# Optimization experiments

Hardware: AMD Instinct MI355X
Metric: run time of the kernel (lower is better)

Reference implementation:

```python
import jax, jax.numpy as jnp
import numpy as np
from jax import lax

NLAT_IN, NLON_IN = 480, 960
NLAT_OUT, NLON_OUT = 721, 1440
KSIZE = 9      # morlet basis: prod(kernel_shape) = 3*3
NNZ = 20       # sparse quadrature entries per output latitude row
C_IN, C_OUT = 32, 32
BATCH = 1


def setup_inputs() -> dict:
    key = jax.random.key(0)
    k1, k2, k3, k4, k5 = jax.random.split(key, 5)
    x = jax.random.normal(k1, (BATCH, C_IN, NLAT_IN, NLON_IN), dtype=jnp.float32)
    weight = jax.random.normal(k2, (C_OUT, C_IN, KSIZE), dtype=jnp.float32) * 0.05
    # sparse DISCO quadrature values (quadrature weights folded in)
    psi_vals = jax.random.uniform(k3, (KSIZE, NLAT_OUT, NNZ), dtype=jnp.float32) / NNZ
    # geodesic neighborhood: latitude rows within +-2 of output row, small lon offsets
    ho = jnp.arange(NLAT_OUT, dtype=jnp.int32)[:, None]
    psi_hi = jnp.clip(ho + jax.random.randint(k4, (NLAT_OUT, NNZ), -2, 3, dtype=jnp.int32), 0, NLAT_OUT - 1)
    psi_dw = jax.random.randint(k5, (NLAT_OUT, NNZ), -10, 11, dtype=jnp.int32) % NLON_OUT
    return {"x": x, "weight": weight, "psi_vals": psi_vals, "psi_hi": psi_hi, "psi_dw": psi_dw}


def _resample_s2(x, h_out, w_out):
    """Bilinear lat interpolation + periodic linear lon interpolation (ResampleS2)."""
    b, c, h, w = x.shape
    # latitude: both grids are linspace(0, pi, nlat) equiangular
    pos_h = jnp.linspace(0.0, float(h - 1), h_out)
    h0 = jnp.clip(jnp.floor(pos_h).astype(jnp.int32), 0, h - 2)
    fh = (pos_h - h0.astype(jnp.float32)).astype(x.dtype)
    x = x[:, :, h0, :] * (1.0 - fh)[None, None, :, None] + x[:, :, h0 + 1, :] * fh[None, None, :, None]
    # longitude: periodic, lon_j = 2*pi*j/nlon
    pos_w = jnp.arange(w_out, dtype=jnp.float32) * (w / w_out)
    w0 = jnp.floor(pos_w).astype(jnp.int32)
    fw = (pos_w - w0.astype(jnp.float32)).astype(x.dtype)
    w0 = w0 % w
    w1 = (w0 + 1) % w
    return x[..., w0] * (1.0 - fw) + x[..., w1] * fw


def _disco_conv(x, weight, psi_vals, psi_hi, psi_dw):
    """Sparse discrete-continuous spherical conv (gather -> basis weight -> channel mix).
    psi is stored for longitude 0 and applied with a periodic longitude shift."""
    b, c, h, w = x.shape  # [B, Cin, 721, 1440]
    o = weight.shape[0]
    wo = jnp.arange(w, dtype=jnp.int32)

    def body(acc, inp):
        v, hi, dw = inp  # v: [K, Hout], hi/dw: [Hout]
        cols = (dw[:, None] + wo[None, :]) % w          # [Hout, W]
        g = x[:, :, hi[:, None], cols]                  # gather -> [B, Cin, Hout, W]
        weff = jnp.einsum("ock,kh->och", weight, v)     # fold basis into channel mix
        return acc + jnp.einsum("och,bchw->bohw", weff, g), None

    acc0 = jnp.zeros((b, o, h, w), dtype=x.dtype)
    scan_in = (jnp.moveaxis(psi_vals, 2, 0), psi_hi.T, psi_dw.T)  # leading axis NNZ
    acc, _ = lax.scan(body, acc0, scan_in)
    return acc


def reference(x, weight, psi_vals, psi_hi, psi_dw):
    x = _resample_s2(x, NLAT_OUT, NLON_OUT)
    return _disco_conv(x, weight, psi_vals, psi_hi, psi_dw)
```

## Files before the change

kernel.cpp:

```cpp
#include <hip/hip_runtime.h>
#include <hip/hip_bf16.h>

#define NLAT_IN  480
#define NLON_IN  960
#define NLAT_OUT 721
#define NLON_OUT 1440
#define KSIZE    9
#define NNZ      20
#define CH       32

typedef __bf16 bf16x8 __attribute__((ext_vector_type(8)));
typedef float  f32x4  __attribute__((ext_vector_type(4)));
typedef unsigned u32x4 __attribute__((ext_vector_type(4)));

__device__ __forceinline__ unsigned short f2bf(float f) {
    unsigned u = __float_as_uint(f);
    u += 0x7fffu + ((u >> 16) & 1u);
    return (unsigned short)(u >> 16);
}

#define W_TILE   180
#define IN_LD4   31
#define LDS_PITCH 129

__global__ __launch_bounds__(256) void resample_kernel(
        const float* __restrict__ x,
        unsigned short* __restrict__ xr) {
    __shared__ float ld[2 * CH * LDS_PITCH];

    int h  = blockIdx.y;
    int bx = blockIdx.x;
    int wb = bx * W_TILE;
    int base_in = bx * (W_TILE * 2 / 3);

    float pos_h = (float)h * (479.0f / 720.0f);
    int h0 = (int)floorf(pos_h);
    if (h0 < 0) h0 = 0;
    if (h0 > NLAT_IN - 2) h0 = NLAT_IN - 2;
    float fh = pos_h - (float)h0;

    const int t = threadIdx.x;
    for (int i = 0; i < 8; ++i) {
        int lin = i * 256 + t;
        if (lin < 2 * CH * IN_LD4) {
            int r   = lin / (CH * IN_LD4);
            int rem = lin - r * (CH * IN_LD4);
            int c   = rem / IN_LD4;
            int j   = rem - c * IN_LD4;
            int src = base_in + 4 * j;
            if (src >= NLON_IN) src -= NLON_IN;
            f32x4 v = *(const f32x4*)(x + ((size_t)c * NLAT_IN + h0 + r) * NLON_IN + src);
            float* dst = ld + (r * CH + c) * LDS_PITCH + 4 * j;
            dst[0] = v.x; dst[1] = v.y; dst[2] = v.z; dst[3] = v.w;
        }
    }
    __syncthreads();

    float ifh = 1.0f - fh;
    for (int i = 0; i < 3; ++i) {
        int d = i * 256 + t;
        if (d >= W_TILE * (CH / 8)) break;
        int w_l = d >> 2;
        int cg  = d & 3;
        int w = wb + w_l;
        float pos_w = (float)w * ((float)NLON_IN / (float)NLON_OUT);
        int w0 = (int)floorf(pos_w);
        float fw = pos_w - (float)w0;
        int wl0 = w0 - base_in;
        float ifw = 1.0f - fw;

        unsigned rr[4];
#pragma unroll
        for (int j = 0; j < 4; ++j) {
            int c = cg * 8 + j * 2;
            const float* r0 = ld + c * LDS_PITCH + wl0;
            const float* r1 = r0 + CH * LDS_PITCH;
            float v0 = ifh * (ifw * r0[0] + fw * r0[1]) + fh * (ifw * r1[0] + fw * r1[1]);
            const float* q0 = r0 + LDS_PITCH;
            const float* q1 = r1 + LDS_PITCH;
            float v1 = ifh * (ifw * q0[0] + fw * q0[1]) + fh * (ifw * q1[0] + fw * q1[1]);
            rr[j] = (unsigned)f2bf(v0) | ((unsigned)f2bf(v1) << 16);
        }
        u32x4 uv; uv[0] = rr[0]; uv[1] = rr[1]; uv[2] = rr[2]; uv[3] = rr[3];
        *(u32x4*)((unsigned*)xr + ((size_t)h * NLON_OUT + w) * (CH / 2) + cg * 4) = uv;
    }
}

__global__ __launch_bounds__(256) void weff_kernel(
        const float* __restrict__ weight,
        const float* __restrict__ psi_vals,
        unsigned short* __restrict__ weff) {
    __shared__ float wl[KSIZE * CH * CH];

    const int t = threadIdx.x;
    for (int i = 0; i < 9; ++i) {
        int lin = i * 256 + t;
        if (lin < KSIZE * CH * CH / 4) {
            f32x4 v = *(const f32x4*)(weight + lin * 4);
            float vv[4] = {v.x, v.y, v.z, v.w};
#pragma unroll
            for (int q = 0; q < 4; ++q) {
                int l4 = lin * 4 + q;
                int k  = l4 % KSIZE;
                int occ = l4 / KSIZE;
                wl[k * (CH * CH) + occ] = vv[q];
            }
        }
    }
    __syncthreads();

    int hnz = blockIdx.x * 16 + (t >> 4);
    int cp  = t & 15;
    if (hnz >= NLAT_OUT * NNZ) return;

    float p[KSIZE];
#pragma unroll
    for (int k = 0; k < KSIZE; ++k)
        p[k] = psi_vals[(size_t)k * (NLAT_OUT * NNZ) + hnz];

    unsigned* outp = (unsigned*)weff + (size_t)hnz * (CH * CH / 2) + cp;
#pragma unroll 4
    for (int oc = 0; oc < CH; ++oc) {
        float a0 = 0.f, a1 = 0.f;
        const float* wb = wl + oc * CH + cp * 2;
#pragma unroll
        for (int k = 0; k < KSIZE; ++k) {
            a0 += wb[k * (CH * CH)]     * p[k];
            a1 += wb[k * (CH * CH) + 1] * p[k];
        }
        outp[oc * 16] = (unsigned)f2bf(a0) | ((unsigned)f2bf(a1) << 16);
    }
}

#define ST_ROWS 8
#define ST_COLS 128
#define HBLK4   181
#define NPAIRD  (HBLK4 * 15)
#define PER_XCD ((NPAIRD + 7) / 8)

__global__ __launch_bounds__(512, 4) void disco_kernel(
        const unsigned short* __restrict__ xr,
        const unsigned short* __restrict__ weff,
        const int* __restrict__ psi_hi,
        const int* __restrict__ psi_dw,
        float* __restrict__ out) {
    __shared__ unsigned short st[ST_ROWS * ST_COLS * CH];

    int bid = blockIdx.x;
    int xcd = bid & 7;
    int p   = xcd * PER_XCD + (bid >> 3);
    if (p >= NPAIRD) return;
    int hblk = p / 15;
    int wblk = p - hblk * 15;
    int h0        = hblk * 4;
    int wbase_blk = wblk * 96;

    int wave = threadIdx.x >> 6;
    int lane = threadIdx.x & 63;
    int l15  = lane & 15;
    int quad = lane >> 4;
    int c0   = quad * 8;
    int jh   = wave >> 1;
    int wq   = wave & 1;

    int  h  = h0 + jh;
    bool hv = (h < NLAT_OUT);

    int swz = ((lane >> 2) << 5) + (((lane & 3) ^ ((lane >> 3) & 3)) << 3);

    const unsigned short* weff_h = weff + (size_t)h * (NNZ * CH * CH);
    const int* hip_ = psi_hi + h * NNZ;
    const int* dwp  = psi_dw + h * NNZ;

    bf16x8 pa0[2], pa1[2];
    int phi[2], pdw[2];
    if (hv) {
#pragma unroll
        for (int q = 0; q < 2; ++q) {
            const unsigned short* wp = weff_h + q * (CH * CH);
            pa0[q] = *(const bf16x8*)(wp + l15 * CH + c0);
            pa1[q] = *(const bf16x8*)(wp + (16 + l15) * CH + c0);
            phi[q] = hip_[q];
            pdw[q] = dwp[q];
        }
    }

    int cstart = wbase_blk - 16;
    if (cstart < 0) cstart += NLON_OUT;
    for (int i = wave; i < ST_ROWS * (ST_COLS / 16); i += 8) {
        int r  = i >> 3;
        int ck = i & 7;
        int gh = h0 - 2 + r;
        gh = gh < 0 ? 0 : (gh > NLAT_OUT - 1 ? NLAT_OUT - 1 : gh);
        int gc = cstart + ck * 16;
        if (gc >= NLON_OUT) gc -= NLON_OUT;
        const unsigned short* gp = xr + ((size_t)gh * NLON_OUT + gc) * CH + swz;
        unsigned short* lp = st + (r * ST_COLS + ck * 16) * CH;
        __builtin_amdgcn_global_load_lds(
            (const __attribute__((address_space(1))) void*)gp,
            (__attribute__((address_space(3))) void*)lp, 16, 0, 0);
    }
    __syncthreads();

    if (hv) {
        f32x4 acc[2][3] = {};
        int wcol0 = 16 + wq * 48 + l15;

#pragma unroll
        for (int nz = 0; nz < NNZ; ++nz) {
            const int sl = nz & 1;
            bf16x8 a0 = pa0[sl];
            bf16x8 a1 = pa1[sl];
            int hi = phi[sl];
            int dw = pdw[sl];
            if (nz + 2 < NNZ) {
                const unsigned short* wp = weff_h + (nz + 2) * (CH * CH);
                pa0[sl] = *(const bf16x8*)(wp + l15 * CH + c0);
                pa1[sl] = *(const bf16x8*)(wp + (16 + l15) * CH + c0);
                phi[sl] = hip_[nz + 2];
                pdw[sl] = dwp[nz + 2];
            }
            int shift = dw > 720 ? dw - NLON_OUT : dw;
            int rloc  = hi - h0 + 2;
            int cbase = wcol0 + shift;
            int sel   = ((((cbase >> 1) & 3) ^ quad) << 3);
            const unsigned short* bp =
                st + (size_t)rloc * (ST_COLS * CH) + cbase * CH + sel;
#pragma unroll
            for (int s = 0; s < 3; ++s) {
                bf16x8 b = *(const bf16x8*)(bp + s * 16 * CH);
                acc[0][s] = __builtin_amdgcn_mfma_f32_16x16x32_bf16(a0, b, acc[0][s], 0, 0, 0);
                acc[1][s] = __builtin_amdgcn_mfma_f32_16x16x32_bf16(a1, b, acc[1][s], 0, 0, 0);
            }
        }

#pragma unroll
        for (int hh = 0; hh < 2; ++hh)
#pragma unroll
            for (int s = 0; s < 3; ++s)
#pragma unroll
                for (int r = 0; r < 4; ++r) {
                    int oc = hh * 16 + quad * 4 + r;
                    int w  = wbase_blk + wq * 48 + s * 16 + l15;
                    out[((size_t)oc * NLAT_OUT + h) * NLON_OUT + w] = acc[hh][s][r];
                }
    }
}

extern "C" void kernel_launch(void* const* d_in, const int* in_sizes, int n_in,
                              void* d_out, int out_size, void* d_ws, size_t ws_size,
                              hipStream_t stream) {
    const float* x        = (const float*)d_in[0];
    const float* weight   = (const float*)d_in[1];
    const float* psi_vals = (const float*)d_in[2];
    const int*   psi_hi   = (const int*)d_in[3];
    const int*   psi_dw   = (const int*)d_in[4];
    float* out = (float*)d_out;

    unsigned short* xr = (unsigned short*)d_ws;
    unsigned short* wf = (unsigned short*)((char*)d_ws + (size_t)NLAT_OUT * NLON_OUT * CH * 2);

    {
        dim3 grid(NLON_OUT / W_TILE, NLAT_OUT);
        resample_kernel<<<grid, 256, 0, stream>>>(x, xr);
    }
    {
        int nblk = (NLAT_OUT * NNZ + 15) / 16;
        weff_kernel<<<nblk, 256, 0, stream>>>(weight, psi_vals, wf);
    }
    {
        disco_kernel<<<8 * PER_XCD, 512, 0, stream>>>(xr, wf, psi_hi, psi_dw, out);
    }
}
```

Measured before the change: 305.6 us.

## Merge resample and weff kernels; shrink disco tile to 48 columns with deeper prefetch

Merges the resample and weff precompute kernels into one launch, with block-index ranges selecting the role. This removes one kernel launch and its tail. The disco kernel now uses 256-thread blocks that each cover 48 longitude columns and 4 latitude rows, with a smaller 80-column LDS stage, so there are more, smaller blocks. The weff/psi register prefetch depth goes from 2 to 4 and is issued before the barrier so it overlaps the LDS fill. The cost is more halo reloading per output column (80 staged columns for 48 outputs instead of 128 for 96) and higher register pressure.

```diff
diff --git a/kernel.cpp b/kernel.cpp
--- a/kernel.cpp
+++ b/kernel.cpp
@@ -22,14 +22,66 @@
 #define W_TILE   180
 #define IN_LD4   31
 #define LDS_PITCH 129
-
-__global__ __launch_bounds__(256) void resample_kernel(
+#define NBLK_WEFF 902
+#define NBLK_RES  (8 * NLAT_OUT)
+
+__global__ __launch_bounds__(256) void pre_kernel(
         const float* __restrict__ x,
-        unsigned short* __restrict__ xr) {
-    __shared__ float ld[2 * CH * LDS_PITCH];
-
-    int h  = blockIdx.y;
-    int bx = blockIdx.x;
+        const float* __restrict__ weight,
+        const float* __restrict__ psi_vals,
+        unsigned short* __restrict__ xr,
+        unsigned short* __restrict__ weff) {
+    __shared__ float smem[KSIZE * CH * CH];
+
+    const int bid = blockIdx.x;
+    const int t   = threadIdx.x;
+
+    if (bid < NBLK_WEFF) {
+        float* wl = smem;
+        for (int i = 0; i < 9; ++i) {
+            int lin = i * 256 + t;
+            if (lin < KSIZE * CH * CH / 4) {
+                f32x4 v = *(const f32x4*)(weight + lin * 4);
+                float vv[4] = {v.x, v.y, v.z, v.w};
+#pragma unroll
+                for (int q = 0; q < 4; ++q) {
+                    int l4 = lin * 4 + q;
+                    int k  = l4 % KSIZE;
+                    int occ = l4 / KSIZE;
+                    wl[k * (CH * CH) + occ] = vv[q];
+                }
+            }
+        }
+        __syncthreads();
+
+        int hnz = bid * 16 + (t >> 4);
+        int cp  = t & 15;
+        if (hnz >= NLAT_OUT * NNZ) return;
+
+        float p[KSIZE];
+#pragma unroll
+        for (int k = 0; k < KSIZE; ++k)
+            p[k] = psi_vals[(size_t)k * (NLAT_OUT * NNZ) + hnz];
+
+        unsigned* outp = (unsigned*)weff + (size_t)hnz * (CH * CH / 2) + cp;
+#pragma unroll 4
+        for (int oc = 0; oc < CH; ++oc) {
+            float a0 = 0.f, a1 = 0.f;
+            const float* wb = wl + oc * CH + cp * 2;
+#pragma unroll
+            for (int k = 0; k < KSIZE; ++k) {
+                a0 += wb[k * (CH * CH)]     * p[k];
+                a1 += wb[k * (CH * CH) + 1] * p[k];
+            }
+            outp[oc * 16] = (unsigned)f2bf(a0) | ((unsigned)f2bf(a1) << 16);
+        }
+        return;
+    }
+
+    float* ld = smem;
+    int bid2 = bid - NBLK_WEFF;
+    int bx = bid2 & 7;
+    int h  = bid2 >> 3;
     int wb = bx * W_TILE;
     int base_in = bx * (W_TILE * 2 / 3);
 
@@ -39,7 +91,6 @@
     if (h0 > NLAT_IN - 2) h0 = NLAT_IN - 2;
     float fh = pos_h - (float)h0;
 
-    const int t = threadIdx.x;
     for (int i = 0; i < 8; ++i) {
         int lin = i * 256 + t;
         if (lin < 2 * CH * IN_LD4) {
@@ -86,59 +137,15 @@
     }
 }
 
-__global__ __launch_bounds__(256) void weff_kernel(
-        const float* __restrict__ weight,
-        const float* __restrict__ psi_vals,
-        unsigned short* __restrict__ weff) {
-    __shared__ float wl[KSIZE * CH * CH];
-
-    const int t = threadIdx.x;
-    for (int i = 0; i < 9; ++i) {
-        int lin = i * 256 + t;
-        if (lin < KSIZE * CH * CH / 4) {
-            f32x4 v = *(const f32x4*)(weight + lin * 4);
-            float vv[4] = {v.x, v.y, v.z, v.w};
-#pragma unroll
-            for (int q = 0; q < 4; ++q) {
-                int l4 = lin * 4 + q;
-                int k  = l4 % KSIZE;
-                int occ = l4 / KSIZE;
-                wl[k * (CH * CH) + occ] = vv[q];
-            }
-        }
-    }
-    __syncthreads();
-
-    int hnz = blockIdx.x * 16 + (t >> 4);
-    int cp  = t & 15;
-    if (hnz >= NLAT_OUT * NNZ) return;
-
-    float p[KSIZE];
-#pragma unroll
-    for (int k = 0; k < KSIZE; ++k)
-        p[k] = psi_vals[(size_t)k * (NLAT_OUT * NNZ) + hnz];
-
-    unsigned* outp = (unsigned*)weff + (size_t)hnz * (CH * CH / 2) + cp;
-#pragma unroll 4
-    for (int oc = 0; oc < CH; ++oc) {
-        float a0 = 0.f, a1 = 0.f;
-        const float* wb = wl + oc * CH + cp * 2;
-#pragma unroll
-        for (int k = 0; k < KSIZE; ++k) {
-            a0 += wb[k * (CH * CH)]     * p[k];
-            a1 += wb[k * (CH * CH) + 1] * p[k];
-        }
-        outp[oc * 16] = (unsigned)f2bf(a0) | ((unsigned)f2bf(a1) << 16);
-    }
-}
-
 #define ST_ROWS 8
-#define ST_COLS 128
+#define ST_COLS 80
+#define WC      48
 #define HBLK4   181
-#define NPAIRD  (HBLK4 * 15)
+#define NWBLK   (NLON_OUT / WC)
+#define NPAIRD  (HBLK4 * NWBLK)
 #define PER_XCD ((NPAIRD + 7) / 8)
 
-__global__ __launch_bounds__(512, 4) void disco_kernel(
+__global__ __launch_bounds__(256, 4) void disco_kernel(
         const unsigned short* __restrict__ xr,
         const unsigned short* __restrict__ weff,
         const int* __restrict__ psi_hi,
@@ -150,46 +157,27 @@
     int xcd = bid & 7;
     int p   = xcd * PER_XCD + (bid >> 3);
     if (p >= NPAIRD) return;
-    int hblk = p / 15;
-    int wblk = p - hblk * 15;
+    int hblk = p / NWBLK;
+    int wblk = p - hblk * NWBLK;
     int h0        = hblk * 4;
-    int wbase_blk = wblk * 96;
+    int wbase_blk = wblk * WC;
 
     int wave = threadIdx.x >> 6;
     int lane = threadIdx.x & 63;
     int l15  = lane & 15;
     int quad = lane >> 4;
     int c0   = quad * 8;
-    int jh   = wave >> 1;
-    int wq   = wave & 1;
-
-    int  h  = h0 + jh;
+
+    int  h  = h0 + wave;
     bool hv = (h < NLAT_OUT);
 
     int swz = ((lane >> 2) << 5) + (((lane & 3) ^ ((lane >> 3) & 3)) << 3);
-
-    const unsigned short* weff_h = weff + (size_t)h * (NNZ * CH * CH);
-    const int* hip_ = psi_hi + h * NNZ;
-    const int* dwp  = psi_dw + h * NNZ;
-
-    bf16x8 pa0[2], pa1[2];
-    int phi[2], pdw[2];
-    if (hv) {
-#pragma unroll
-        for (int q = 0; q < 2; ++q) {
-            const unsigned short* wp = weff_h + q * (CH * CH);
-            pa0[q] = *(const bf16x8*)(wp + l15 * CH + c0);
-            pa1[q] = *(const bf16x8*)(wp + (16 + l15) * CH + c0);
-            phi[q] = hip_[q];
-            pdw[q] = dwp[q];
-        }
-    }
 
     int cstart = wbase_blk - 16;
     if (cstart < 0) cstart += NLON_OUT;
-    for (int i = wave; i < ST_ROWS * (ST_COLS / 16); i += 8) {
-        int r  = i >> 3;
-        int ck = i & 7;
+    for (int i = wave; i < ST_ROWS * (ST_COLS / 16); i += 4) {
+        int r  = i / 5;
+        int ck = i - r * 5;
         int gh = h0 - 2 + r;
         gh = gh < 0 ? 0 : (gh > NLAT_OUT - 1 ? NLAT_OUT - 1 : gh);
         int gc = cstart + ck * 16;
@@ -200,25 +188,42 @@
             (const __attribute__((address_space(1))) void*)gp,
             (__attribute__((address_space(3))) void*)lp, 16, 0, 0);
     }
+
+    const unsigned short* weff_h = weff + (size_t)h * (NNZ * CH * CH);
+    const int* hip_ = psi_hi + h * NNZ;
+    const int* dwp  = psi_dw + h * NNZ;
+
+    bf16x8 pa0[4], pa1[4];
+    int phi[4], pdw[4];
+    if (hv) {
+#pragma unroll
+        for (int q = 0; q < 4; ++q) {
+            const unsigned short* wp = weff_h + q * (CH * CH);
+            pa0[q] = *(const bf16x8*)(wp + l15 * CH + c0);
+            pa1[q] = *(const bf16x8*)(wp + (16 + l15) * CH + c0);
+            phi[q] = hip_[q];
+            pdw[q] = dwp[q];
+        }
+    }
     __syncthreads();
 
     if (hv) {
         f32x4 acc[2][3] = {};
-        int wcol0 = 16 + wq * 48 + l15;
+        int wcol0 = 16 + l15;
 
 #pragma unroll
         for (int nz = 0; nz < NNZ; ++nz) {
-            const int sl = nz & 1;
+            const int sl = nz & 3;
             bf16x8 a0 = pa0[sl];
             bf16x8 a1 = pa1[sl];
             int hi = phi[sl];
             int dw = pdw[sl];
-            if (nz + 2 < NNZ) {
-                const unsigned short* wp = weff_h + (nz + 2) * (CH * CH);
+            if (nz + 4 < NNZ) {
+                const unsigned short* wp = weff_h + (nz + 4) * (CH * CH);
                 pa0[sl] = *(const bf16x8*)(wp + l15 * CH + c0);
                 pa1[sl] = *(const bf16x8*)(wp + (16 + l15) * CH + c0);
-                phi[sl] = hip_[nz + 2];
-                pdw[sl] = dwp[nz + 2];
+                phi[sl] = hip_[nz + 4];
+                pdw[sl] = dwp[nz + 4];
             }
             int shift = dw > 720 ? dw - NLON_OUT : dw;
             int rloc  = hi - h0 + 2;
@@ -241,7 +246,7 @@
 #pragma unroll
                 for (int r = 0; r < 4; ++r) {
                     int oc = hh * 16 + quad * 4 + r;
-                    int w  = wbase_blk + wq * 48 + s * 16 + l15;
+                    int w  = wbase_blk + s * 16 + l15;
                     out[((size_t)oc * NLAT_OUT + h) * NLON_OUT + w] = acc[hh][s][r];
                 }
     }
@@ -261,14 +266,9 @@
     unsigned short* wf = (unsigned short*)((char*)d_ws + (size_t)NLAT_OUT * NLON_OUT * CH * 2);
 
     {
-        dim3 grid(NLON_OUT / W_TILE, NLAT_OUT);
-        resample_kernel<<<grid, 256, 0, stream>>>(x, xr);
+        pre_kernel<<<NBLK_WEFF + NBLK_RES, 256, 0, stream>>>(x, weight, psi_vals, xr, wf);
     }
     {
-        int nblk = (NLAT_OUT * NNZ + 15) / 16;
-        weff_kernel<<<nblk, 256, 0, stream>>>(weight, psi_vals, wf);
-    }
-    {
-        disco_kernel<<<8 * PER_XCD, 512, 0, stream>>>(xr, wf, psi_hi, psi_dw, out);
-    }
-}
+        disco_kernel<<<8 * PER_XCD, 256, 0, stream>>>(xr, wf, psi_hi, psi_dw, out);
+    }
+}
```

Measured after the change: 304.3 us. No clear change (-0.4%).
